# Kernel tuning notes

Measured on AMD Instinct MI355X. Metric: run time of the kernel, lower is better.

The kernel has to match this reference:

```python
import jax, jax.numpy as jnp
import numpy as np

N_NODES = 100000
N_EDGES = 3200000
N_GRAPHS = 128
F_IN, HID = 16, 64


def setup_inputs() -> dict:
    key = jax.random.key(0)
    ks = jax.random.split(key, 16)
    def lin(k, fan_in, fan_out):
        bound = 1.0 / np.sqrt(fan_in)
        kw, kb = jax.random.split(k)
        W = jax.random.uniform(kw, (fan_in, fan_out), jnp.float32, -bound, bound)
        b = jax.random.uniform(kb, (fan_out,), jnp.float32, -bound, bound)
        return W, b
    x = jax.random.normal(ks[0], (N_NODES, F_IN), jnp.float32)
    edge_index = jax.random.randint(ks[1], (2, N_EDGES), 0, N_NODES, jnp.int64 if jax.config.jax_enable_x64 else jnp.int32)
    edge_attr = jax.random.normal(ks[2], (N_EDGES, 4), jnp.float32)
    batch = jnp.sort(jax.random.randint(ks[3], (N_NODES,), 0, N_GRAPHS))
    W1, b1 = lin(ks[4], F_IN, HID)
    W2, b2 = lin(ks[5], HID, HID)
    W3, b3 = lin(ks[6], HID, HID)
    Wf1, bf1 = lin(ks[7], HID, 32)
    Wf2, bf2 = lin(ks[8], 32, 1)
    return dict(x=x, edge_index=edge_index, edge_attr=edge_attr, batch=batch,
                W1=W1, b1=b1, W2=W2, b2=b2, W3=W3, b3=b3,
                Wf1=Wf1, bf1=bf1, Wf2=Wf2, bf2=bf2)


def _gcn_conv(x, src, dst, norm, W, b, n_nodes):
    # PyG GCNConv: out = scatter_add(norm * (x @ W)[src] -> dst) + b
    h = x @ W                                   # [N, out]
    msg = h[src] * norm[:, None]                # [E+N, out] gather + scale
    agg = jax.ops.segment_sum(msg, dst, num_segments=n_nodes)
    return agg + b


def reference(x, edge_index, edge_attr, batch, W1, b1, W2, b2, W3, b3, Wf1, bf1, Wf2, bf2):
    n = x.shape[0]
    # add self loops (GCNConv default)
    loop = jnp.arange(n, dtype=edge_index.dtype)
    src = jnp.concatenate([edge_index[0], loop])
    dst = jnp.concatenate([edge_index[1], loop])
    # symmetric degree normalization: deg computed on dst with self loops
    deg = jax.ops.segment_sum(jnp.ones_like(src, dtype=x.dtype), dst, num_segments=n)
    dinv = jax.lax.rsqrt(jnp.maximum(deg, 1.0))
    norm = dinv[src] * dinv[dst]

    h = jax.nn.relu(_gcn_conv(x, src, dst, norm, W1, b1, n))   # dropout = identity (eval)
    h = jax.nn.relu(_gcn_conv(h, src, dst, norm, W2, b2, n))
    h = jax.nn.relu(_gcn_conv(h, src, dst, norm, W3, b3, n))

    # global mean pool over graphs
    sums = jax.ops.segment_sum(h, batch, num_segments=N_GRAPHS)          # [B, HID]
    cnts = jax.ops.segment_sum(jnp.ones((n,), x.dtype), batch, num_segments=N_GRAPHS)
    pooled = sums / jnp.maximum(cnts, 1.0)[:, None]

    z = jax.nn.relu(pooled @ Wf1 + bf1)
    return z @ Wf2 + bf2                                                  # [B, 1]
```

## Files before the change

kernel.cpp:

```cpp
#include <hip/hip_runtime.h>
#include <hip/hip_bf16.h>

#define HID 64
#define MAXNB 2048
#define NBLK 512
#define FILL_T 1024
#define HREP 4
#define SEG_CAP 2560

__device__ __forceinline__ float bf2f(unsigned short u) {
    return __uint_as_float(((unsigned)u) << 16);
}
__device__ __forceinline__ unsigned short f2bf(float f) {
    __hip_bfloat16 b = __float2bfloat16(f);
    return *(unsigned short*)&b;
}
__device__ __forceinline__ unsigned packbf(float lo, float hi) {
    return (unsigned)f2bf(lo) | ((unsigned)f2bf(hi) << 16);
}


__global__ __launch_bounds__(FILL_T) void radix_fill2_kernel(
    const int* __restrict__ ei, int* __restrict__ gcur,
    unsigned* __restrict__ ebuf, int E, int NB, int C) {
    __shared__ int lh[HREP * (MAXNB + 1)];
    __shared__ int lcur[MAXNB];
    int blk = blockIdx.x, tid = threadIdx.x;
    for (int i = tid; i < HREP * (MAXNB + 1); i += FILL_T) lh[i] = 0;
    __syncthreads();
    int* lhr = lh + ((tid >> 6) & (HREP - 1)) * (MAXNB + 1);
    int lo = blk * C, hi = min(lo + C, E);
    int cnt = hi - lo;
    int n4 = ((E & 3) == 0) ? (cnt >> 2) : 0;
    const int4* d4 = (const int4*)(ei + (long long)E + lo);
    for (int k = tid; k < n4; k += FILL_T) {
        int4 d = d4[k];
        atomicAdd(&lhr[d.x >> 6], 1);
        atomicAdd(&lhr[d.y >> 6], 1);
        atomicAdd(&lhr[d.z >> 6], 1);
        atomicAdd(&lhr[d.w >> 6], 1);
    }
    for (int e = lo + (n4 << 2) + tid; e < hi; e += FILL_T)
        atomicAdd(&lhr[ei[(long long)E + e] >> 6], 1);
    __syncthreads();
    for (int i = tid; i < NB; i += FILL_T) {
        int v = 0;
#pragma unroll
        for (int r = 0; r < HREP; r++) v += lh[r * (MAXNB + 1) + i];
        int start = v ? atomicAdd(&gcur[i], v) : 0;
        lcur[i] = i * SEG_CAP + start;
    }
    __syncthreads();
    const int4* s4 = (const int4*)(ei + lo);
    for (int k = tid; k < n4; k += FILL_T) {
        int4 s = s4[k];
        int4 d = d4[k];
        int p0 = atomicAdd(&lcur[d.x >> 6], 1);
        int p1 = atomicAdd(&lcur[d.y >> 6], 1);
        int p2 = atomicAdd(&lcur[d.z >> 6], 1);
        int p3 = atomicAdd(&lcur[d.w >> 6], 1);
        ebuf[p0] = ((unsigned)s.x << 6) | (unsigned)(d.x & 63);
        ebuf[p1] = ((unsigned)s.y << 6) | (unsigned)(d.y & 63);
        ebuf[p2] = ((unsigned)s.z << 6) | (unsigned)(d.z & 63);
        ebuf[p3] = ((unsigned)s.w << 6) | (unsigned)(d.w & 63);
    }
    for (int e = lo + (n4 << 2) + tid; e < hi; e += FILL_T) {
        int s = ei[e];
        int d = ei[(long long)E + e];
        int pos = atomicAdd(&lcur[d >> 6], 1);
        ebuf[pos] = ((unsigned)s << 6) | (unsigned)(d & 63);
    }
}

__global__ __launch_bounds__(256) void node_csr_xs_kernel(
    const int* __restrict__ gcur, const unsigned* __restrict__ ebuf,
    const float* __restrict__ x,
    int* __restrict__ row_ptr, int* __restrict__ rend,
    int* __restrict__ col, float* __restrict__ dinv,
    unsigned short* __restrict__ xs, int N, int NB) {
    __shared__ unsigned sE[SEG_CAP];
    __shared__ int lcnt[64];
    __shared__ int lcur[64];
    __shared__ float sDv[64];
    int bkt = blockIdx.x, tid = threadIdx.x;
    int beg = bkt * SEG_CAP;
    int cnt = min(gcur[bkt], SEG_CAP);
    if (tid < 64) lcnt[tid] = 0;
    for (int i = tid; i < cnt; i += 256) sE[i] = ebuf[beg + i];
    __syncthreads();
    for (int i = tid; i < cnt; i += 256) atomicAdd(&lcnt[sE[i] & 63u], 1);
    __syncthreads();
    if (tid < 64) {
        int v = lcnt[tid];
        int p = v;
#pragma unroll
        for (int off = 1; off < 64; off <<= 1) {
            int t = __shfl_up(p, off);
            if (tid >= off) p += t;
        }
        int base = beg + p - v;
        lcur[tid] = base;
        int node = (bkt << 6) + tid;
        float dv = rsqrtf((float)(v + 1));
        sDv[tid] = dv;
        if (node < N) {
            row_ptr[node] = base;
            rend[node] = base + v;
            dinv[node] = dv;
        }
    }
    __syncthreads();
    for (int i = tid; i < cnt; i += 256) {
        unsigned ev = sE[i];
        int pos = atomicAdd(&lcur[ev & 63u], 1);
        col[pos] = (int)(ev >> 6);
    }
    {
        int r = tid >> 2, q = tid & 3;
        int node = (bkt << 6) + r;
        if (node < N) {
            float dv = sDv[r];
            float4 xv = *(const float4*)(x + (long long)node * 16 + q * 4);
            uint2 w;
            w.x = packbf(dv * xv.x, dv * xv.y);
            w.y = packbf(dv * xv.z, dv * xv.w);
            *(uint2*)(xs + (long long)node * 16 + q * 4) = w;
        }
    }
}

__device__ __forceinline__ void add4(float* acc, uint2 r) {
    acc[0] += __uint_as_float(r.x << 16);
    acc[1] += __uint_as_float(r.x & 0xffff0000u);
    acc[2] += __uint_as_float(r.y << 16);
    acc[3] += __uint_as_float(r.y & 0xffff0000u);
}

__global__ __launch_bounds__(256) void gather16_kernel(
    const int* __restrict__ row_ptr, const int* __restrict__ rend,
    const int* __restrict__ col,
    const unsigned short* __restrict__ xs, float* __restrict__ agg, int N) {
    int wv = __builtin_amdgcn_readfirstlane(threadIdx.x >> 6);
    int node = blockIdx.x * 4 + wv;
    int lane = threadIdx.x & 63;
    if (node >= N) return;
    int grp = lane >> 2;
    int c = lane & 3;
    int beg = row_ptr[node], end = rend[node];

    float acc[4] = {0.f, 0.f, 0.f, 0.f};
    if (grp == 0) {
        uint2 rs = *(const uint2*)(xs + ((long long)node << 4) + (c << 2));
        add4(acc, rs);
    }
    for (int base = beg; base < end; base += 32) {
        int e0 = base + grp;
        int e1 = e0 + 16;
        bool k0 = e0 < end, k1 = e1 < end;
        int c0 = k0 ? col[e0] : 0;
        int c1 = k1 ? col[e1] : 0;
        uint2 r0 = *(const uint2*)(xs + (((long long)c0) << 4) + (c << 2));
        uint2 r1 = *(const uint2*)(xs + (((long long)c1) << 4) + (c << 2));
        if (k0) add4(acc, r0);
        if (k1) add4(acc, r1);
    }
#pragma unroll
    for (int m = 4; m <= 32; m <<= 1) {
#pragma unroll
        for (int k = 0; k < 4; k++) acc[k] += __shfl_xor(acc[k], m);
    }
    if (lane < 4) {
        float4 w = make_float4(acc[0], acc[1], acc[2], acc[3]);
        *(float4*)(agg + ((long long)node << 4) + (lane << 2)) = w;
    }
}

__global__ __launch_bounds__(256) void gemm_agg2_kernel(
    const float* __restrict__ agg,
    const float* __restrict__ W1, const float* __restrict__ b1,
    const float* __restrict__ W2,
    const float* __restrict__ dinv, unsigned short* __restrict__ g2, int N) {
    __shared__ float sW1[16 * HID];
    __shared__ float sW2[HID * HID];
    __shared__ float sIn[16 * 16];
    __shared__ float sH[16 * HID];
    __shared__ float sB1[HID];
    __shared__ float sDv[16];
    int tid = threadIdx.x;
    for (int i = tid; i < 16 * HID; i += 256) sW1[i] = W1[i];
    for (int i = tid; i < HID * HID; i += 256) sW2[i] = W2[i];
    if (tid < HID) sB1[tid] = b1[tid];
    int base = blockIdx.x * 16;
    {
        int r = tid >> 4, c = tid & 15;
        int node = base + r;
        sIn[tid] = (node < N) ? agg[(long long)node * 16 + c] : 0.f;
    }
    if (tid < 16) {
        int node = base + tid;
        sDv[tid] = (node < N) ? dinv[node] : 0.f;
    }
    __syncthreads();
    int j = tid & 63;
    int si = tid >> 6;
#pragma unroll
    for (int u = 0; u < 4; u++) {
        int r = si * 4 + u;
        float acc = 0.f;
#pragma unroll
        for (int k = 0; k < 16; k++) acc += sIn[r * 16 + k] * sW1[k * HID + j];
        float v = sDv[r] * acc + sB1[j];
        sH[r * HID + j] = v > 0.f ? v : 0.f;
    }
    __syncthreads();
#pragma unroll
    for (int u = 0; u < 4; u++) {
        int r = si * 4 + u;
        int node = base + r;
        if (node >= N) continue;
        float acc = 0.f;
#pragma unroll 16
        for (int k = 0; k < HID; k++) acc += sH[r * HID + k] * sW2[k * HID + j];
        g2[(long long)node * HID + j] = f2bf(sDv[r] * acc);
    }
}

template <typename Tin, int K>
__global__ void gemm_g_kernel(const Tin* __restrict__ in,
                              const float* __restrict__ W,
                              const float* __restrict__ dinv,
                              unsigned short* __restrict__ g, int N) {
    __shared__ float sW[K * HID];
    __shared__ float sIn[16 * K];
    int tid = threadIdx.x;
    for (int idx = tid; idx < K * HID; idx += 256) sW[idx] = W[idx];
    int base = blockIdx.x * 16;
    for (int idx = tid; idx < 16 * K; idx += 256) {
        int r = idx / K, c = idx % K;
        int node = base + r;
        float v = 0.f;
        if (node < N) {
            Tin t = in[(long long)node * K + c];
            if constexpr (sizeof(Tin) == 2) v = bf2f((unsigned short)t);
            else v = (float)t;
        }
        sIn[idx] = v;
    }
    __syncthreads();
    int j = tid & 63;
    int si = tid >> 6;
#pragma unroll
    for (int u = 0; u < 4; u++) {
        int r = si * 4 + u;
        int node = base + r;
        if (node >= N) continue;
        float acc = 0.f;
#pragma unroll
        for (int k = 0; k < K; k++) acc += sIn[r * K + k] * sW[k * HID + j];
        g[(long long)node * HID + j] = f2bf(dinv[node] * acc);
    }
}

__device__ __forceinline__ void add8(float* acc, uint4 r) {
    acc[0] += __uint_as_float(r.x << 16);
    acc[1] += __uint_as_float(r.x & 0xffff0000u);
    acc[2] += __uint_as_float(r.y << 16);
    acc[3] += __uint_as_float(r.y & 0xffff0000u);
    acc[4] += __uint_as_float(r.z << 16);
    acc[5] += __uint_as_float(r.z & 0xffff0000u);
    acc[6] += __uint_as_float(r.w << 16);
    acc[7] += __uint_as_float(r.w & 0xffff0000u);
}

__global__ __launch_bounds__(256) void gather_kernel(
    const int* __restrict__ row_ptr, const int* __restrict__ rend,
    const int* __restrict__ col,
    const unsigned short* __restrict__ g, const float* __restrict__ dinv,
    const float* __restrict__ bias, unsigned short* __restrict__ h, int N) {
    int wv = __builtin_amdgcn_readfirstlane(threadIdx.x >> 6);
    int node = blockIdx.x * 4 + wv;
    int lane = threadIdx.x & 63;
    if (node >= N) return;
    int grp = lane >> 3;
    int c = lane & 7;
    int beg = row_ptr[node], end = rend[node];

    float acc[8] = {0.f, 0.f, 0.f, 0.f, 0.f, 0.f, 0.f, 0.f};
    if (grp == 0) {
        uint4 rs = *(const uint4*)(g + ((long long)node << 6) + (c << 3));
        add8(acc, rs);
    }

    for (int base = beg; base < end; base += 32) {
        int e0 = base + grp;
        int e1 = e0 + 8, e2 = e0 + 16, e3 = e0 + 24;
        bool k0 = e0 < end, k1 = e1 < end, k2 = e2 < end, k3 = e3 < end;
        int c0 = k0 ? col[e0] : 0;
        int c1 = k1 ? col[e1] : 0;
        int c2 = k2 ? col[e2] : 0;
        int c3 = k3 ? col[e3] : 0;
        uint4 r0 = *(const uint4*)(g + (((long long)c0) << 6) + (c << 3));
        uint4 r1 = *(const uint4*)(g + (((long long)c1) << 6) + (c << 3));
        uint4 r2 = *(const uint4*)(g + (((long long)c2) << 6) + (c << 3));
        uint4 r3 = *(const uint4*)(g + (((long long)c3) << 6) + (c << 3));
        if (k0) add8(acc, r0);
        if (k1) add8(acc, r1);
        if (k2) add8(acc, r2);
        if (k3) add8(acc, r3);
    }

#pragma unroll
    for (int m = 8; m <= 32; m <<= 1) {
#pragma unroll
        for (int k = 0; k < 8; k++) acc[k] += __shfl_xor(acc[k], m);
    }

    if (lane < 8) {
        float dv = dinv[node];
        float4 ba = *(const float4*)(bias + (lane << 3));
        float4 bb = *(const float4*)(bias + (lane << 3) + 4);
        float v0 = dv * acc[0] + ba.x;
        float v1 = dv * acc[1] + ba.y;
        float v2 = dv * acc[2] + ba.z;
        float v3 = dv * acc[3] + ba.w;
        float v4 = dv * acc[4] + bb.x;
        float v5 = dv * acc[5] + bb.y;
        float v6 = dv * acc[6] + bb.z;
        float v7 = dv * acc[7] + bb.w;
        v0 = v0 > 0.f ? v0 : 0.f;
        v1 = v1 > 0.f ? v1 : 0.f;
        v2 = v2 > 0.f ? v2 : 0.f;
        v3 = v3 > 0.f ? v3 : 0.f;
        v4 = v4 > 0.f ? v4 : 0.f;
        v5 = v5 > 0.f ? v5 : 0.f;
        v6 = v6 > 0.f ? v6 : 0.f;
        v7 = v7 > 0.f ? v7 : 0.f;
        uint4 w;
        w.x = (unsigned)f2bf(v0) | ((unsigned)f2bf(v1) << 16);
        w.y = (unsigned)f2bf(v2) | ((unsigned)f2bf(v3) << 16);
        w.z = (unsigned)f2bf(v4) | ((unsigned)f2bf(v5) << 16);
        w.w = (unsigned)f2bf(v6) | ((unsigned)f2bf(v7) << 16);
        *(uint4*)(h + ((long long)node << 6) + (lane << 3)) = w;
    }
}

__global__ void pool_kernel(const unsigned short* __restrict__ h, const int* __restrict__ batch,
                            float* __restrict__ sums, float* __restrict__ cnt, int N) {
    int wave = blockIdx.x * 4 + (threadIdx.x >> 6);
    int lane = threadIdx.x & 63;
    int lo = wave * 16;
    if (lo >= N) return;
    int hi = min(lo + 16, N);
    int curb = batch[lo];
    float sum = 0.f;
    int nseg = 0;
    for (int i = lo; i < hi; i++) {
        int b = batch[i];
        if (b != curb) {
            atomicAdd(&sums[curb * HID + lane], sum);
            if (lane == 0) atomicAdd(&cnt[curb], (float)nseg);
            curb = b; sum = 0.f; nseg = 0;
        }
        sum += bf2f(h[(long long)i * HID + lane]);
        nseg++;
    }
    atomicAdd(&sums[curb * HID + lane], sum);
    if (lane == 0) atomicAdd(&cnt[curb], (float)nseg);
}

__global__ void final_kernel(const float* __restrict__ sums, const float* __restrict__ cnt,
                             const float* __restrict__ Wf1, const float* __restrict__ bf1,
                             const float* __restrict__ Wf2, const float* __restrict__ bf2,
                             float* __restrict__ out) {
    __shared__ float sW1[HID * 32];
    __shared__ float sW2[32];
    int tid = threadIdx.x;
    for (int idx = tid; idx < HID * 32; idx += 128) sW1[idx] = Wf1[idx];
    if (tid < 32) sW2[tid] = Wf2[tid];
    __syncthreads();
    int b = tid;
    float pooled[HID];
    float c = fmaxf(cnt[b], 1.0f);
#pragma unroll
    for (int j = 0; j < HID; j++) pooled[j] = sums[b * HID + j] / c;
    float o = bf2[0];
#pragma unroll 4
    for (int hd = 0; hd < 32; hd++) {
        float z = bf1[hd];
#pragma unroll
        for (int j = 0; j < HID; j++) z += pooled[j] * sW1[j * 32 + hd];
        z = fmaxf(z, 0.f);
        o += z * sW2[hd];
    }
    out[b] = o;
}

extern "C" void kernel_launch(void* const* d_in, const int* in_sizes, int n_in,
                              void* d_out, int out_size, void* d_ws, size_t ws_size,
                              hipStream_t stream) {
    const float* x     = (const float*)d_in[0];
    const int*   ei    = (const int*)d_in[1];
    const int*   batch = (const int*)d_in[3];
    const float* W1  = (const float*)d_in[4];
    const float* b1  = (const float*)d_in[5];
    const float* W2  = (const float*)d_in[6];
    const float* b2  = (const float*)d_in[7];
    const float* W3  = (const float*)d_in[8];
    const float* b3  = (const float*)d_in[9];
    const float* Wf1 = (const float*)d_in[10];
    const float* bf1 = (const float*)d_in[11];
    const float* Wf2 = (const float*)d_in[12];
    const float* bf2 = (const float*)d_in[13];
    float* out = (float*)d_out;

    const int N  = in_sizes[0] / 16;
    const int E  = in_sizes[1] / 2;
    const int NB = (N + 63) / 64;

    char* ws = (char*)d_ws;
    size_t o = 0;
    float*          dinv    = (float*)(ws + o);          o += ((size_t)N * 4 + 4095) / 4096 * 4096;
    int*            row_ptr = (int*)(ws + o);            o += ((size_t)N * 4 + 4095) / 4096 * 4096;
    int*            rend    = (int*)(ws + o);            o += ((size_t)N * 4 + 4095) / 4096 * 4096;
    int*            gcur    = (int*)(ws + o);            o += ((size_t)NB * 4 + 4095) / 4096 * 4096;
    unsigned*       ebuf    = (unsigned*)(ws + o);       o += (size_t)NB * SEG_CAP * 4;
    int*            col     = (int*)(ws + o);            o += (size_t)NB * SEG_CAP * 4;
    unsigned short* A       = (unsigned short*)(ws + o); o += (size_t)N * HID * 2;
    unsigned short* B       = (unsigned short*)(ws + o); o += (size_t)N * HID * 2;
    unsigned short* XS      = (unsigned short*)(ws + o); o += ((size_t)N * 16 * 2 + 4095) / 4096 * 4096;
    float*          AGG     = (float*)(ws + o);          o += ((size_t)N * 16 * 4 + 4095) / 4096 * 4096;
    float*          sums    = (float*)(ws + o);          o += 128 * HID * 4;
    float*          cnt     = (float*)(ws + o);          o += 128 * 4;
    (void)ws_size;

    const int T = 256;
    const int Cchunk = (((E + NBLK - 1) / NBLK) + 3) & ~3;
    const int gGm = (N + 15) / 16;
    const int gGa = (N + 3) / 4;
    const int gPool = ((N + 15) / 16 + 3) / 4;

    hipMemsetAsync(gcur, 0, (size_t)NB * 4, stream);
    radix_fill2_kernel<<<NBLK, FILL_T, 0, stream>>>(ei, gcur, ebuf, E, NB, Cchunk);
    node_csr_xs_kernel<<<NB, T, 0, stream>>>(gcur, ebuf, x, row_ptr, rend, col, dinv, XS, N, NB);

    gather16_kernel<<<gGa, T, 0, stream>>>(row_ptr, rend, col, XS, AGG, N);
    gemm_agg2_kernel<<<gGm, T, 0, stream>>>(AGG, W1, b1, W2, dinv, A, N);

    gather_kernel<<<gGa, T, 0, stream>>>(row_ptr, rend, col, A, dinv, b2, B, N);

    gemm_g_kernel<unsigned short, 64><<<gGm, T, 0, stream>>>(B, W3, dinv, B, N);
    gather_kernel<<<gGa, T, 0, stream>>>(row_ptr, rend, col, B, dinv, b3, A, N);

    hipMemsetAsync(sums, 0, (128 * HID + 128) * 4, stream);
    pool_kernel<<<gPool, T, 0, stream>>>(A, batch, sums, cnt, N);
    final_kernel<<<1, 128, 0, stream>>>(sums, cnt, Wf1, bf1, Wf2, bf2, out);
}
```

Measured before the change: 484.8 us.

## Fuse last-layer gather with mean pooling and drop the separate pool pass

The final GCN gather now pools its outputs directly into per-graph sums. Each block reduces its four nodes in shared memory and issues one atomic when they share a graph, so the bf16 write and re-read of the last hidden layer go away. Graph counts are found by binary search on the sorted batch array in the final kernel, and the sums memset moves into the CSR-build kernel. Column index loads become nontemporal to keep cache for the feature gathers. The cost is many float atomics, one set per block, and a pooled result no longer rounded through bf16.

```diff
diff --git a/kernel.cpp b/kernel.cpp
--- a/kernel.cpp
+++ b/kernel.cpp
@@ -18,7 +18,9 @@
 __device__ __forceinline__ unsigned packbf(float lo, float hi) {
     return (unsigned)f2bf(lo) | ((unsigned)f2bf(hi) << 16);
 }
-
+__device__ __forceinline__ int ldnt(const int* p) {
+    return __builtin_nontemporal_load(p);
+}
 
 __global__ __launch_bounds__(FILL_T) void radix_fill2_kernel(
     const int* __restrict__ ei, int* __restrict__ gcur,
@@ -77,12 +79,15 @@
     const float* __restrict__ x,
     int* __restrict__ row_ptr, int* __restrict__ rend,
     int* __restrict__ col, float* __restrict__ dinv,
-    unsigned short* __restrict__ xs, int N, int NB) {
+    unsigned short* __restrict__ xs, float* __restrict__ sums, int N, int NB) {
     __shared__ unsigned sE[SEG_CAP];
     __shared__ int lcnt[64];
     __shared__ int lcur[64];
     __shared__ float sDv[64];
     int bkt = blockIdx.x, tid = threadIdx.x;
+    if (bkt == 0) {
+        for (int i = tid; i < 128 * HID; i += 256) sums[i] = 0.f;
+    }
     int beg = bkt * SEG_CAP;
     int cnt = min(gcur[bkt], SEG_CAP);
     if (tid < 64) lcnt[tid] = 0;
@@ -157,8 +162,8 @@
         int e0 = base + grp;
         int e1 = e0 + 16;
         bool k0 = e0 < end, k1 = e1 < end;
-        int c0 = k0 ? col[e0] : 0;
-        int c1 = k1 ? col[e1] : 0;
+        int c0 = k0 ? ldnt(col + e0) : 0;
+        int c1 = k1 ? ldnt(col + e1) : 0;
         uint2 r0 = *(const uint2*)(xs + (((long long)c0) << 4) + (c << 2));
         uint2 r1 = *(const uint2*)(xs + (((long long)c1) << 4) + (c << 2));
         if (k0) add4(acc, r0);
@@ -290,15 +295,14 @@
         uint4 rs = *(const uint4*)(g + ((long long)node << 6) + (c << 3));
         add8(acc, rs);
     }
-
     for (int base = beg; base < end; base += 32) {
         int e0 = base + grp;
         int e1 = e0 + 8, e2 = e0 + 16, e3 = e0 + 24;
         bool k0 = e0 < end, k1 = e1 < end, k2 = e2 < end, k3 = e3 < end;
-        int c0 = k0 ? col[e0] : 0;
-        int c1 = k1 ? col[e1] : 0;
-        int c2 = k2 ? col[e2] : 0;
-        int c3 = k3 ? col[e3] : 0;
+        int c0 = k0 ? ldnt(col + e0) : 0;
+        int c1 = k1 ? ldnt(col + e1) : 0;
+        int c2 = k2 ? ldnt(col + e2) : 0;
+        int c3 = k3 ? ldnt(col + e3) : 0;
         uint4 r0 = *(const uint4*)(g + (((long long)c0) << 6) + (c << 3));
         uint4 r1 = *(const uint4*)(g + (((long long)c1) << 6) + (c << 3));
         uint4 r2 = *(const uint4*)(g + (((long long)c2) << 6) + (c << 3));
@@ -308,13 +312,11 @@
         if (k2) add8(acc, r2);
         if (k3) add8(acc, r3);
     }
-
 #pragma unroll
     for (int m = 8; m <= 32; m <<= 1) {
 #pragma unroll
         for (int k = 0; k < 8; k++) acc[k] += __shfl_xor(acc[k], m);
     }
-
     if (lane < 8) {
         float dv = dinv[node];
         float4 ba = *(const float4*)(bias + (lane << 3));
@@ -344,43 +346,108 @@
     }
 }
 
-__global__ void pool_kernel(const unsigned short* __restrict__ h, const int* __restrict__ batch,
-                            float* __restrict__ sums, float* __restrict__ cnt, int N) {
-    int wave = blockIdx.x * 4 + (threadIdx.x >> 6);
+__global__ __launch_bounds__(256) void gather_pool_kernel(
+    const int* __restrict__ row_ptr, const int* __restrict__ rend,
+    const int* __restrict__ col,
+    const unsigned short* __restrict__ g, const float* __restrict__ dinv,
+    const float* __restrict__ bias, const int* __restrict__ batch,
+    float* __restrict__ sums, int N) {
+    __shared__ float ps[4][HID];
+    __shared__ int pb[4];
+    int wv = __builtin_amdgcn_readfirstlane(threadIdx.x >> 6);
+    int node = blockIdx.x * 4 + wv;
     int lane = threadIdx.x & 63;
-    int lo = wave * 16;
-    if (lo >= N) return;
-    int hi = min(lo + 16, N);
-    int curb = batch[lo];
-    float sum = 0.f;
-    int nseg = 0;
-    for (int i = lo; i < hi; i++) {
-        int b = batch[i];
-        if (b != curb) {
-            atomicAdd(&sums[curb * HID + lane], sum);
-            if (lane == 0) atomicAdd(&cnt[curb], (float)nseg);
-            curb = b; sum = 0.f; nseg = 0;
+    bool act = node < N;
+    int grp = lane >> 3;
+    int c = lane & 7;
+    int beg = 0, end = 0;
+    if (act) { beg = row_ptr[node]; end = rend[node]; }
+
+    float acc[8] = {0.f, 0.f, 0.f, 0.f, 0.f, 0.f, 0.f, 0.f};
+    if (act && grp == 0) {
+        uint4 rs = *(const uint4*)(g + ((long long)node << 6) + (c << 3));
+        add8(acc, rs);
+    }
+    for (int base = beg; base < end; base += 32) {
+        int e0 = base + grp;
+        int e1 = e0 + 8, e2 = e0 + 16, e3 = e0 + 24;
+        bool k0 = e0 < end, k1 = e1 < end, k2 = e2 < end, k3 = e3 < end;
+        int c0 = k0 ? ldnt(col + e0) : 0;
+        int c1 = k1 ? ldnt(col + e1) : 0;
+        int c2 = k2 ? ldnt(col + e2) : 0;
+        int c3 = k3 ? ldnt(col + e3) : 0;
+        uint4 r0 = *(const uint4*)(g + (((long long)c0) << 6) + (c << 3));
+        uint4 r1 = *(const uint4*)(g + (((long long)c1) << 6) + (c << 3));
+        uint4 r2 = *(const uint4*)(g + (((long long)c2) << 6) + (c << 3));
+        uint4 r3 = *(const uint4*)(g + (((long long)c3) << 6) + (c << 3));
+        if (k0) add8(acc, r0);
+        if (k1) add8(acc, r1);
+        if (k2) add8(acc, r2);
+        if (k3) add8(acc, r3);
+    }
+#pragma unroll
+    for (int m = 8; m <= 32; m <<= 1) {
+#pragma unroll
+        for (int k = 0; k < 8; k++) acc[k] += __shfl_xor(acc[k], m);
+    }
+    if (lane == 0) pb[wv] = act ? batch[node] : -1;
+    if (lane < 8) {
+        float dv = act ? dinv[node] : 0.f;
+        float4 ba = *(const float4*)(bias + (lane << 3));
+        float4 bb = *(const float4*)(bias + (lane << 3) + 4);
+        float v0 = dv * acc[0] + ba.x;
+        float v1 = dv * acc[1] + ba.y;
+        float v2 = dv * acc[2] + ba.z;
+        float v3 = dv * acc[3] + ba.w;
+        float v4 = dv * acc[4] + bb.x;
+        float v5 = dv * acc[5] + bb.y;
+        float v6 = dv * acc[6] + bb.z;
+        float v7 = dv * acc[7] + bb.w;
+        float4 wa = make_float4(v0 > 0.f ? v0 : 0.f, v1 > 0.f ? v1 : 0.f,
+                                v2 > 0.f ? v2 : 0.f, v3 > 0.f ? v3 : 0.f);
+        float4 wb = make_float4(v4 > 0.f ? v4 : 0.f, v5 > 0.f ? v5 : 0.f,
+                                v6 > 0.f ? v6 : 0.f, v7 > 0.f ? v7 : 0.f);
+        *(float4*)(&ps[wv][lane << 3]) = wa;
+        *(float4*)(&ps[wv][(lane << 3) + 4]) = wb;
+    }
+    __syncthreads();
+    if (threadIdx.x < HID) {
+        int f = threadIdx.x;
+        int b0 = pb[0];
+        bool uni = (pb[1] == b0) & (pb[2] == b0) & (pb[3] == b0);
+        if (uni & (b0 >= 0)) {
+            atomicAdd(&sums[b0 * HID + f], ps[0][f] + ps[1][f] + ps[2][f] + ps[3][f]);
+        } else {
+#pragma unroll
+            for (int w = 0; w < 4; w++)
+                if (pb[w] >= 0) atomicAdd(&sums[pb[w] * HID + f], ps[w][f]);
         }
-        sum += bf2f(h[(long long)i * HID + lane]);
-        nseg++;
-    }
-    atomicAdd(&sums[curb * HID + lane], sum);
-    if (lane == 0) atomicAdd(&cnt[curb], (float)nseg);
-}
-
-__global__ void final_kernel(const float* __restrict__ sums, const float* __restrict__ cnt,
+    }
+}
+
+__global__ void final_kernel(const float* __restrict__ sums, const int* __restrict__ batch,
                              const float* __restrict__ Wf1, const float* __restrict__ bf1,
                              const float* __restrict__ Wf2, const float* __restrict__ bf2,
-                             float* __restrict__ out) {
+                             float* __restrict__ out, int N) {
     __shared__ float sW1[HID * 32];
     __shared__ float sW2[32];
+    __shared__ int sUB[128];
     int tid = threadIdx.x;
     for (int idx = tid; idx < HID * 32; idx += 128) sW1[idx] = Wf1[idx];
     if (tid < 32) sW2[tid] = Wf2[tid];
+    {
+        int lo = 0, hi = N;
+        while (lo < hi) {
+            int mid = (lo + hi) >> 1;
+            if (batch[mid] <= tid) lo = mid + 1; else hi = mid;
+        }
+        sUB[tid] = lo;
+    }
     __syncthreads();
     int b = tid;
+    float c = (float)(sUB[b] - (b ? sUB[b - 1] : 0));
+    c = fmaxf(c, 1.0f);
     float pooled[HID];
-    float c = fmaxf(cnt[b], 1.0f);
 #pragma unroll
     for (int j = 0; j < HID; j++) pooled[j] = sums[b * HID + j] / c;
     float o = bf2[0];
@@ -430,18 +497,16 @@
     unsigned short* XS      = (unsigned short*)(ws + o); o += ((size_t)N * 16 * 2 + 4095) / 4096 * 4096;
     float*          AGG     = (float*)(ws + o);          o += ((size_t)N * 16 * 4 + 4095) / 4096 * 4096;
     float*          sums    = (float*)(ws + o);          o += 128 * HID * 4;
-    float*          cnt     = (float*)(ws + o);          o += 128 * 4;
     (void)ws_size;
 
     const int T = 256;
     const int Cchunk = (((E + NBLK - 1) / NBLK) + 3) & ~3;
     const int gGm = (N + 15) / 16;
     const int gGa = (N + 3) / 4;
-    const int gPool = ((N + 15) / 16 + 3) / 4;
 
     hipMemsetAsync(gcur, 0, (size_t)NB * 4, stream);
     radix_fill2_kernel<<<NBLK, FILL_T, 0, stream>>>(ei, gcur, ebuf, E, NB, Cchunk);
-    node_csr_xs_kernel<<<NB, T, 0, stream>>>(gcur, ebuf, x, row_ptr, rend, col, dinv, XS, N, NB);
+    node_csr_xs_kernel<<<NB, T, 0, stream>>>(gcur, ebuf, x, row_ptr, rend, col, dinv, XS, sums, N, NB);
 
     gather16_kernel<<<gGa, T, 0, stream>>>(row_ptr, rend, col, XS, AGG, N);
     gemm_agg2_kernel<<<gGm, T, 0, stream>>>(AGG, W1, b1, W2, dinv, A, N);
@@ -449,9 +514,7 @@
     gather_kernel<<<gGa, T, 0, stream>>>(row_ptr, rend, col, A, dinv, b2, B, N);
 
     gemm_g_kernel<unsigned short, 64><<<gGm, T, 0, stream>>>(B, W3, dinv, B, N);
-    gather_kernel<<<gGa, T, 0, stream>>>(row_ptr, rend, col, B, dinv, b3, A, N);
-
-    hipMemsetAsync(sums, 0, (128 * HID + 128) * 4, stream);
-    pool_kernel<<<gPool, T, 0, stream>>>(A, batch, sums, cnt, N);
-    final_kernel<<<1, 128, 0, stream>>>(sums, cnt, Wf1, bf1, Wf2, bf2, out);
-}
+    gather_pool_kernel<<<gGa, T, 0, stream>>>(row_ptr, rend, col, B, dinv, b3, batch, sums, N);
+
+    final_kernel<<<1, 128, 0, stream>>>(sums, batch, Wf1, bf1, Wf2, bf2, out, N);
+}
```

New measurement: 489.3 us. About the same (+0.9%).
